# Performance work log

Measured on AMD Instinct MI355X. Metric: run time of the kernel, lower is better.

## Reference

```python
import jax, jax.numpy as jnp
import numpy as np
import math

B, N, D = 2, 4096, 1024
H, R, M = 16, 4, 8
BUCKET = 64

def setup_inputs() -> dict:
    key = jax.random.key(0)
    k1, k2, k3, k4, k5 = jax.random.split(key, 5)
    d = D // H
    return {
        "query": jax.random.normal(k1, (B, N, D), jnp.float32),
        "key": jax.random.normal(k2, (B, N, D), jnp.float32),
        "value": jax.random.normal(k3, (B, N, D), jnp.float32),
        "valence": jax.random.uniform(k4, (B,), jnp.float32),
        "hash_projections": jax.random.normal(k5, (R, H, d, M), jnp.float32),
        "valence_scale": jnp.ones((1,), jnp.float32),
    }

def reference(query, key, value, valence, hash_projections, valence_scale):
    b, n, dm = query.shape
    h = H
    d = dm // h
    r, _, _, m = hash_projections.shape
    c = n // BUCKET  # n_buckets (must divide exactly, matching torch view)
    # (B,N,D) -> (B,H,N,d)
    Q = query.reshape(b, n, h, d).transpose(0, 2, 1, 3)
    K = key.reshape(b, n, h, d).transpose(0, 2, 1, 3)
    V = value.reshape(b, n, h, d).transpose(0, 2, 1, 3)
    # LSH hash: argmax over M random projections per round -> (B,R,H,N)
    hashes = jnp.einsum('bhnd,rhdm->brhnm', Q, hash_projections)
    codes = jnp.argmax(hashes, axis=-1)
    # valence modulation (torch: scale.long().clamp(1, M); int truncation)
    scale = 1.0 + valence_scale[0] * valence.mean()
    scale_i = jnp.clip(scale.astype(jnp.int32), 1, m)
    codes = codes * scale_i
    # sort positions by hash code per (B,R,H)
    idx = jnp.argsort(codes, axis=-1)  # (B,R,H,N)
    idx_e = idx[..., None]  # (B,R,H,N,1), broadcasts over d
    K_sorted = jnp.take_along_axis(K[:, None], idx_e, axis=3)  # (B,R,H,N,d)
    V_sorted = jnp.take_along_axis(V[:, None], idx_e, axis=3)
    Kb = K_sorted.reshape(b, r, h, c, BUCKET, d)
    Vb = V_sorted.reshape(b, r, h, c, BUCKET, d)
    # NOTE: queries are bucketed in ORIGINAL order (faithful to source)
    Qb = Q.reshape(b, h, c, BUCKET, d)
    scores = jnp.einsum('bhcsd,brhced->brhcse', Qb, Kb) / math.sqrt(d)
    attn = jax.nn.softmax(scores, axis=-1)  # (B,R,H,C,S,E)
    outb = jnp.einsum('brhcse,brhced->brhcsd', attn, Vb)
    out = outb.reshape(b, r, h, n, d).mean(axis=1)  # average over hash rounds
    out = out.transpose(0, 2, 1, 3).reshape(b, n, dm)  # dropout is identity (eval)
    return out, attn.mean(axis=(1, 2))
```

## Files before the change

kernel.cpp:

```cpp
#include <hip/hip_runtime.h>
#include <hip/hip_bf16.h>

#define BB 2
#define NN 4096
#define DD 1024
#define HH 16
#define RR 4
#define MM 8
#define CC 64
#define DH 64
#define PAD 68

typedef __attribute__((ext_vector_type(8))) short bf16x8;
typedef __attribute__((ext_vector_type(8))) unsigned short ushort8;
typedef __attribute__((ext_vector_type(4))) float f32x4;
typedef unsigned long long u64;

__device__ __forceinline__ unsigned short f2bf(float x) {
  union { __hip_bfloat16 b; unsigned short u; } cv;
  cv.b = __float2bfloat16(x);
  return cv.u;
}
__device__ __forceinline__ int swz(int row, int colbyte) {
  return row * 128 + (colbyte ^ ((row & 7) << 4));
}
__device__ __forceinline__ bf16x8 pack8(float4 a, float4 b, float sc) {
  bf16x8 r;
  const float* pa = (const float*)&a;
  const float* pb = (const float*)&b;
#pragma unroll
  for (int j = 0; j < 4; ++j) {
    r[j] = (short)f2bf(pa[j] * sc);
    r[j + 4] = (short)f2bf(pb[j] * sc);
  }
  return r;
}
__device__ __forceinline__ void load_lds16(const void* g, void* l) {
  __builtin_amdgcn_global_load_lds(
      (const __attribute__((address_space(1))) unsigned*)g,
      (__attribute__((address_space(3))) unsigned*)l, 16, 0, 0);
}

__global__ __launch_bounds__(256) void k_cvt(const float* __restrict__ kmat,
                                             const float* __restrict__ vmat,
                                             unsigned short* __restrict__ kbf,
                                             unsigned short* __restrict__ vbf) {
  int bid = blockIdx.x;
  int b = bid >> 8;
  int n0 = (bid & 255) * 16;
  int tid = threadIdx.x;
  int h = tid >> 4, d4 = tid & 15;
#pragma unroll 4
  for (int it = 0; it < 16; ++it) {
    int row = n0 + it;
    size_t src = (size_t)(b * NN + row) * DD + tid * 4;
    float4 kv = *(const float4*)(kmat + src);
    float4 vv = *(const float4*)(vmat + src);
    size_t dst = ((size_t)(b * HH + h) * NN + row) * 64 + d4 * 4;
    const float* kf = (const float*)&kv;
    const float* vf = (const float*)&vv;
    u64 kp = (u64)f2bf(kf[0]) | ((u64)f2bf(kf[1]) << 16) |
             ((u64)f2bf(kf[2]) << 32) | ((u64)f2bf(kf[3]) << 48);
    u64 vp = (u64)f2bf(vf[0]) | ((u64)f2bf(vf[1]) << 16) |
             ((u64)f2bf(vf[2]) << 32) | ((u64)f2bf(vf[3]) << 48);
    *(u64*)(kbf + dst) = kp;
    *(u64*)(vbf + dst) = vp;
  }
}

__global__ __launch_bounds__(256) void k_hash(const float* __restrict__ q,
                                              const float* __restrict__ proj,
                                              int* __restrict__ codes) {
  int blk = blockIdx.x;
  int nc = blk & (CC - 1);
  int h = (blk >> 6) & (HH - 1);
  int b = blk >> 10;
  __shared__ float Qs[64][PAD];
  __shared__ float Ps[DH][MM];
  __shared__ float Ss[64][9];
  int tid = threadIdx.x;
  const float* qbase = q + ((size_t)(b * NN + nc * 64) * DD + h * DH);
  for (int f = tid; f < 1024; f += 256) {
    int row = f >> 4, c4 = f & 15;
    *(float4*)&Qs[row][c4 * 4] = *(const float4*)(qbase + (size_t)row * DD + c4 * 4);
  }
  int nl = tid >> 3, m = tid & 7;
  for (int r = 0; r < RR; ++r) {
    const float* pbase = proj + (size_t)(r * HH + h) * DH * MM;
    for (int f = tid; f < DH * MM / 4; f += 256)
      ((float4*)Ps)[f] = ((const float4*)pbase)[f];
    __syncthreads();
    float s0 = 0.f, s1 = 0.f;
#pragma unroll
    for (int kk = 0; kk < DH; ++kk) {
      float p = Ps[kk][m];
      s0 += Qs[nl][kk] * p;
      s1 += Qs[nl + 32][kk] * p;
    }
    Ss[nl][m] = s0;
    Ss[nl + 32][m] = s1;
    __syncthreads();
    if (tid < 64) {
      float best = Ss[tid][0];
      int bm = 0;
#pragma unroll
      for (int mm = 1; mm < MM; ++mm) {
        float vv = Ss[tid][mm];
        if (vv > best) { best = vv; bm = mm; }
      }
      codes[(size_t)((b * RR + r) * HH + h) * NN + nc * 64 + tid] = bm;
    }
    __syncthreads();
  }
}

__global__ __launch_bounds__(256) void k_sort(const int* __restrict__ codes,
                                              int* __restrict__ idxo) {
  int gblk = blockIdx.x;
  const int* cg = codes + (size_t)gblk * NN;
  int* ig = idxo + (size_t)gblk * NN;
  int tid = threadIdx.x, lane = tid & 63, w = tid >> 6;
  __shared__ u64 wtot[4][2];
  int myc[16];
#pragma unroll
  for (int qd = 0; qd < 4; ++qd) {
    int4 t4 = ((const int4*)(cg + tid * 16))[qd];
    myc[qd * 4 + 0] = t4.x; myc[qd * 4 + 1] = t4.y;
    myc[qd * 4 + 2] = t4.z; myc[qd * 4 + 3] = t4.w;
  }
  u64 c01 = 0, c23 = 0;
#pragma unroll
  for (int i = 0; i < 16; ++i) {
    int k = myc[i];
    u64 one = 1ull << (16 * (k & 3));
    if (k < 4) c01 += one; else c23 += one;
  }
  u64 i01 = c01, i23 = c23;
#pragma unroll
  for (int d = 1; d < 64; d <<= 1) {
    u64 t0 = __shfl_up(i01, d);
    u64 t1 = __shfl_up(i23, d);
    if (lane >= d) { i01 += t0; i23 += t1; }
  }
  if (lane == 63) { wtot[w][0] = i01; wtot[w][1] = i23; }
  __syncthreads();
  u64 base01 = 0, base23 = 0, g01 = 0, g23 = 0;
#pragma unroll
  for (int ww = 0; ww < 4; ++ww) {
    u64 a = wtot[ww][0], bq = wtot[ww][1];
    if (ww < w) { base01 += a; base23 += bq; }
    g01 += a; g23 += bq;
  }
  u64 p01 = g01 + (g01 << 16); p01 += (p01 << 32);
  u64 p23 = g23 + (g23 << 16); p23 += (p23 << 32);
  u64 cb01 = p01 << 16;
  u64 tot01 = (p01 >> 48) & 0xffffull;
  u64 cb23 = (p23 << 16) + tot01 * 0x0001000100010001ull;
  u64 o01 = cb01 + base01 + (i01 - c01);
  u64 o23 = cb23 + base23 + (i23 - c23);
#pragma unroll
  for (int i = 0; i < 16; ++i) {
    int k = myc[i];
    int sh = 16 * (k & 3);
    int off;
    if (k < 4) { off = (int)((o01 >> sh) & 0xffffull); o01 += 1ull << sh; }
    else       { off = (int)((o23 >> sh) & 0xffffull); o23 += 1ull << sh; }
    ig[off] = tid * 16 + i;
  }
}

__global__ __launch_bounds__(256, 4) void k_attn(const float* __restrict__ q,
                                                 const unsigned short* __restrict__ kbf,
                                                 const unsigned short* __restrict__ vbf,
                                                 const int* __restrict__ idxs,
                                                 float* __restrict__ out,
                                                 float* __restrict__ attn_part,
                                                 float* __restrict__ attn_out,
                                                 int atomic_attn) {
  __shared__ __align__(16) char KB[2][8192];
  __shared__ __align__(16) char VT[8192];
  __shared__ __align__(16) char PL[8192];
  __shared__ int sidx[RR][64];

  int bid = blockIdx.x;
  int blk = (bid & 7) * 256 + (bid >> 3);
  int cblk = blk & 63;
  int h = (blk >> 6) & 15;
  int b = blk >> 10;
  int tid = threadIdx.x;
  int lane = tid & 63;
  int w = tid >> 6;
  int g = lane >> 4;
  int cl = lane & 15;
  int e2 = tid & 31, dg = (tid >> 5) & 7;

  sidx[tid >> 6][tid & 63] =
      idxs[(size_t)((b * RR + (tid >> 6)) * HH + h) * NN + cblk * 64 + (tid & 63)];

  const char* kp = (const char*)(kbf + (size_t)(b * HH + h) * NN * 64);
  const unsigned short* vp = vbf + (size_t)(b * HH + h) * NN * 64;

  const float* qrow = q + (size_t)(b * NN + cblk * 64 + 16 * w + cl) * DD + h * DH;
  bf16x8 qh[2];
#pragma unroll
  for (int ks = 0; ks < 2; ++ks)
    qh[ks] = pack8(*(const float4*)(qrow + 32 * ks + 8 * g),
                   *(const float4*)(qrow + 32 * ks + 8 * g + 4), 0.125f);

  __syncthreads();

  {
    int row = sidx[0][16 * w + cl];
    const char* gs = kp + (size_t)row * 128 + g * 16;
    load_lds16(gs, KB[0] + w * 2048);
    load_lds16(gs + 64, KB[0] + w * 2048 + 1024);
    ushort8 v0r = *(const ushort8*)(vp + (size_t)sidx[0][2 * e2] * 64 + dg * 8);
    ushort8 v1r = *(const ushort8*)(vp + (size_t)sidx[0][2 * e2 + 1] * 64 + dg * 8);
#pragma unroll
    for (int j = 0; j < 8; ++j) {
      unsigned pk = (unsigned)(unsigned short)v0r[j] |
                    ((unsigned)(unsigned short)v1r[j] << 16);
      *(unsigned*)(VT + swz(8 * dg + j, 4 * e2)) = pk;
    }
  }
  __syncthreads();

  f32x4 acc_o[4];
  float attA[4][4];
#pragma unroll
  for (int t = 0; t < 4; ++t) {
    acc_o[t] = (f32x4){0.f, 0.f, 0.f, 0.f};
#pragma unroll
    for (int i = 0; i < 4; ++i) attA[t][i] = 0.f;
  }

#pragma unroll
  for (int r = 0; r < RR; ++r) {
    ushort8 n0r, n1r;
    if (r < RR - 1) {
      int row = sidx[r + 1][16 * w + cl];
      const char* gs = kp + (size_t)row * 128 + g * 16;
      load_lds16(gs, KB[(r + 1) & 1] + w * 2048);
      load_lds16(gs + 64, KB[(r + 1) & 1] + w * 2048 + 1024);
      n0r = *(const ushort8*)(vp + (size_t)sidx[r + 1][2 * e2] * 64 + dg * 8);
      n1r = *(const ushort8*)(vp + (size_t)sidx[r + 1][2 * e2 + 1] * 64 + dg * 8);
    }

    f32x4 s4[4];
#pragma unroll
    for (int t = 0; t < 4; ++t) s4[t] = (f32x4){0.f, 0.f, 0.f, 0.f};
    __builtin_amdgcn_s_setprio(1);
#pragma unroll
    for (int t = 0; t < 4; ++t)
#pragma unroll
      for (int ks = 0; ks < 2; ++ks) {
        bf16x8 kf = *(const bf16x8*)(KB[r & 1] + t * 2048 + ks * 1024 + g * 256 + cl * 16);
        s4[t] = __builtin_amdgcn_mfma_f32_16x16x32_bf16(kf, qh[ks], s4[t], 0, 0, 0);
      }
    __builtin_amdgcn_s_setprio(0);

    {
      f32x4 m4 = s4[0];
#pragma unroll
      for (int t = 1; t < 4; ++t)
#pragma unroll
        for (int i = 0; i < 4; ++i) m4[i] = fmaxf(m4[i], s4[t][i]);
      float mx = fmaxf(fmaxf(m4[0], m4[1]), fmaxf(m4[2], m4[3]));
      mx = fmaxf(mx, __shfl_xor(mx, 16));
      mx = fmaxf(mx, __shfl_xor(mx, 32));
      float sm = 0.f;
#pragma unroll
      for (int t = 0; t < 4; ++t)
#pragma unroll
        for (int i = 0; i < 4; ++i) {
          float e = __expf(s4[t][i] - mx);
          s4[t][i] = e;
          sm += e;
        }
      sm += __shfl_xor(sm, 16);
      sm += __shfl_xor(sm, 32);
      float inv = __builtin_amdgcn_rcpf(sm);
#pragma unroll
      for (int t = 0; t < 4; ++t)
#pragma unroll
        for (int i = 0; i < 4; ++i) {
          s4[t][i] *= inv;
          attA[t][i] += s4[t][i];
        }
    }

#pragma unroll
    for (int t = 0; t < 4; ++t) {
      u64 pk = (u64)f2bf(s4[t][0]) | ((u64)f2bf(s4[t][1]) << 16) |
               ((u64)f2bf(s4[t][2]) << 32) | ((u64)f2bf(s4[t][3]) << 48);
      *(u64*)(PL + w * 2048 + swz(cl, 32 * t + 8 * g)) = pk;
    }
    bf16x8 pa[2];
#pragma unroll
    for (int ks = 0; ks < 2; ++ks)
      pa[ks] = *(const bf16x8*)(PL + w * 2048 + swz(cl, 64 * ks + 16 * g));

    __builtin_amdgcn_s_setprio(1);
#pragma unroll
    for (int t = 0; t < 4; ++t)
#pragma unroll
      for (int ks = 0; ks < 2; ++ks) {
        bf16x8 vt = *(const bf16x8*)(VT + swz(16 * t + cl, ks * 64 + g * 16));
        acc_o[t] = __builtin_amdgcn_mfma_f32_16x16x32_bf16(vt, pa[ks], acc_o[t], 0, 0, 0);
      }
    __builtin_amdgcn_s_setprio(0);

    if (r < RR - 1) {
      __syncthreads();
#pragma unroll
      for (int j = 0; j < 8; ++j) {
        unsigned pk = (unsigned)(unsigned short)n0r[j] |
                      ((unsigned)(unsigned short)n1r[j] << 16);
        *(unsigned*)(VT + swz(8 * dg + j, 4 * e2)) = pk;
      }
      __syncthreads();
    }
  }

  int srow = 16 * w + cl;
  size_t ob = (size_t)(b * NN + cblk * 64 + srow) * DD + h * DH + 4 * g;
#pragma unroll
  for (int t = 0; t < 4; ++t) {
    float4 o = make_float4(acc_o[t][0] * 0.25f, acc_o[t][1] * 0.25f,
                           acc_o[t][2] * 0.25f, acc_o[t][3] * 0.25f);
    *(float4*)(out + ob + 16 * t) = o;
  }
  size_t ab = (((size_t)(b * HH + h) * CC + cblk) * 64 + srow) * 64 + 4 * g;
  if (atomic_attn) {
    const float sc = 1.f / (RR * HH);
    size_t abase = (((size_t)b * CC + cblk) * 64 + srow) * 64 + 4 * g;
#pragma unroll
    for (int t = 0; t < 4; ++t)
#pragma unroll
      for (int i = 0; i < 4; ++i)
        atomicAdd(attn_out + abase + 16 * t + i, attA[t][i] * sc);
  } else {
#pragma unroll
    for (int t = 0; t < 4; ++t) {
      float4 o = make_float4(attA[t][0], attA[t][1], attA[t][2], attA[t][3]);
      *(float4*)(attn_part + ab + 16 * t) = o;
    }
  }
}

__global__ __launch_bounds__(256) void k_attn_reduce(const float* __restrict__ part,
                                                     float* __restrict__ attn_out) {
  size_t o = (size_t)blockIdx.x * 256 + threadIdx.x;
  int se = (int)(o & 4095);
  size_t bc = o >> 12;
  int c = (int)(bc & (CC - 1));
  int b = (int)(bc >> 6);
  float s = 0.f;
  const float* p = part + ((size_t)b * HH * CC + c) * 4096 + se;
#pragma unroll
  for (int h = 0; h < HH; ++h) s += p[(size_t)h * CC * 4096];
  attn_out[o] = s * (1.f / (RR * HH));
}

extern "C" void kernel_launch(void* const* d_in, const int* in_sizes, int n_in,
                              void* d_out, int out_size, void* d_ws, size_t ws_size,
                              hipStream_t stream) {
  const float* q = (const float*)d_in[0];
  const float* k = (const float*)d_in[1];
  const float* v = (const float*)d_in[2];
  const float* proj = (const float*)d_in[4];
  float* out = (float*)d_out;
  float* attn_out = out + (size_t)BB * NN * DD;

  const size_t n_codes = (size_t)BB * RR * HH * NN;
  const size_t n_panel = (size_t)BB * HH * NN * 64;
  const size_t n_part  = (size_t)BB * HH * CC * 4096;

  int* codes = (int*)d_ws;
  int* idxs = codes + n_codes;
  unsigned short* kbf = (unsigned short*)(idxs + n_codes);
  unsigned short* vbf = kbf + n_panel;
  float* attn_part = (float*)(vbf + n_panel);

  size_t need_full = n_codes * 8 + n_panel * 4 + n_part * 4;
  int atomic_attn = (ws_size < need_full) ? 1 : 0;
  if (atomic_attn)
    hipMemsetAsync(attn_out, 0, (size_t)BB * CC * 4096 * sizeof(float), stream);

  k_cvt<<<BB * (NN / 16), 256, 0, stream>>>(k, v, kbf, vbf);
  k_hash<<<BB * HH * CC, 256, 0, stream>>>(q, proj, codes);
  k_sort<<<BB * RR * HH, 256, 0, stream>>>(codes, idxs);
  k_attn<<<BB * HH * CC, 256, 0, stream>>>(q, kbf, vbf, idxs, out, attn_part,
                                           attn_out, atomic_attn);
  if (!atomic_attn)
    k_attn_reduce<<<BB * CC * 4096 / 256, 256, 0, stream>>>(attn_part, attn_out);
}
```

Before: 90.70 us.

## Feed P straight from registers into 16x16x16 MFMA and restructure K/V conversion

The attention kernel no longer stages the softmax probabilities through an LDS buffer. It packs them into bf16x4 registers and feeds them directly to 16x16x16 bf16 MFMAs, whose operand layout matches the score accumulator. V transpose reads switch to an 8-byte swizzle to suit the smaller loads. Dropping the PL buffer lowers LDS use and the launch-bounds occupancy hint rises from 4 to 6 blocks. The K/V bf16 conversion kernel is rewritten so each block handles one tensor, with 16-byte stores that loop over heads. The trade-off is twice as many MFMA instructions of half the K depth, plus possible register pressure at the higher occupancy target.

Result: slower. 213.4 us (+135.3%).

```diff
diff --git a/kernel.cpp b/kernel.cpp
--- a/kernel.cpp
+++ b/kernel.cpp
@@ -12,6 +12,7 @@
 #define PAD 68
 
 typedef __attribute__((ext_vector_type(8))) short bf16x8;
+typedef __attribute__((ext_vector_type(4))) short bf16x4;
 typedef __attribute__((ext_vector_type(8))) unsigned short ushort8;
 typedef __attribute__((ext_vector_type(4))) float f32x4;
 typedef unsigned long long u64;
@@ -24,6 +25,9 @@
 __device__ __forceinline__ int swz(int row, int colbyte) {
   return row * 128 + (colbyte ^ ((row & 7) << 4));
 }
+__device__ __forceinline__ int swz8(int row, int colbyte) {
+  return row * 128 + (colbyte ^ ((row & 15) << 3));
+}
 __device__ __forceinline__ bf16x8 pack8(float4 a, float4 b, float sc) {
   bf16x8 r;
   const float* pa = (const float*)&a;
@@ -39,6 +43,17 @@
   __builtin_amdgcn_global_load_lds(
       (const __attribute__((address_space(1))) unsigned*)g,
       (__attribute__((address_space(3))) unsigned*)l, 16, 0, 0);
+}
+__device__ __forceinline__ f32x4 mfma16(bf16x4 a, bf16x4 b, f32x4 c) {
+#if __has_builtin(__builtin_amdgcn_mfma_f32_16x16x16bf16_1k)
+  return __builtin_amdgcn_mfma_f32_16x16x16bf16_1k(a, b, c, 0, 0, 0);
+#elif __has_builtin(__builtin_amdgcn_mfma_f32_16x16x16_bf16)
+  return __builtin_amdgcn_mfma_f32_16x16x16_bf16(a, b, c, 0, 0, 0);
+#else
+  f32x4 d;
+  asm("v_mfma_f32_16x16x16_bf16 %0, %1, %2, %3" : "=v"(d) : "v"(a), "v"(b), "v"(c));
+  return d;
+#endif
 }
 
 __global__ __launch_bounds__(256) void k_cvt(const float* __restrict__ kmat,
@@ -46,25 +61,29 @@
                                              unsigned short* __restrict__ kbf,
                                              unsigned short* __restrict__ vbf) {
   int bid = blockIdx.x;
-  int b = bid >> 8;
-  int n0 = (bid & 255) * 16;
+  int sel = bid >> 8;
+  int rest = bid & 255;
+  int b = rest >> 7;
+  int chunk = rest & 127;
+  const float* src = sel ? vmat : kmat;
+  unsigned short* dst = sel ? vbf : kbf;
   int tid = threadIdx.x;
-  int h = tid >> 4, d4 = tid & 15;
+  int row = chunk * 32 + (tid >> 3), oct = tid & 7;
+  const float* s0 = src + (size_t)(b * NN + row) * DD + oct * 8;
+  unsigned short* d0 = dst + (size_t)b * HH * NN * 64 + (size_t)row * 64 + oct * 8;
 #pragma unroll 4
-  for (int it = 0; it < 16; ++it) {
-    int row = n0 + it;
-    size_t src = (size_t)(b * NN + row) * DD + tid * 4;
-    float4 kv = *(const float4*)(kmat + src);
-    float4 vv = *(const float4*)(vmat + src);
-    size_t dst = ((size_t)(b * HH + h) * NN + row) * 64 + d4 * 4;
-    const float* kf = (const float*)&kv;
-    const float* vf = (const float*)&vv;
-    u64 kp = (u64)f2bf(kf[0]) | ((u64)f2bf(kf[1]) << 16) |
-             ((u64)f2bf(kf[2]) << 32) | ((u64)f2bf(kf[3]) << 48);
-    u64 vp = (u64)f2bf(vf[0]) | ((u64)f2bf(vf[1]) << 16) |
-             ((u64)f2bf(vf[2]) << 32) | ((u64)f2bf(vf[3]) << 48);
-    *(u64*)(kbf + dst) = kp;
-    *(u64*)(vbf + dst) = vp;
+  for (int h = 0; h < HH; ++h) {
+    float4 a = *(const float4*)(s0 + h * 64);
+    float4 c = *(const float4*)(s0 + h * 64 + 4);
+    const float* af = (const float*)&a;
+    const float* cf = (const float*)&c;
+    ushort8 o;
+#pragma unroll
+    for (int j = 0; j < 4; ++j) {
+      o[j] = f2bf(af[j]);
+      o[j + 4] = f2bf(cf[j]);
+    }
+    *(ushort8*)(d0 + (size_t)h * NN * 64) = o;
   }
 }
 
@@ -169,7 +188,7 @@
   }
 }
 
-__global__ __launch_bounds__(256, 4) void k_attn(const float* __restrict__ q,
+__global__ __launch_bounds__(256, 6) void k_attn(const float* __restrict__ q,
                                                  const unsigned short* __restrict__ kbf,
                                                  const unsigned short* __restrict__ vbf,
                                                  const int* __restrict__ idxs,
@@ -179,7 +198,6 @@
                                                  int atomic_attn) {
   __shared__ __align__(16) char KB[2][8192];
   __shared__ __align__(16) char VT[8192];
-  __shared__ __align__(16) char PL[8192];
   __shared__ int sidx[RR][64];
 
   int bid = blockIdx.x;
@@ -220,7 +238,7 @@
     for (int j = 0; j < 8; ++j) {
       unsigned pk = (unsigned)(unsigned short)v0r[j] |
                     ((unsigned)(unsigned short)v1r[j] << 16);
-      *(unsigned*)(VT + swz(8 * dg + j, 4 * e2)) = pk;
+      *(unsigned*)(VT + swz8(8 * dg + j, 4 * e2)) = pk;
     }
   }
   __syncthreads();
@@ -289,25 +307,26 @@
         }
     }
 
+    bf16x4 pb[4];
 #pragma unroll
     for (int t = 0; t < 4; ++t) {
-      u64 pk = (u64)f2bf(s4[t][0]) | ((u64)f2bf(s4[t][1]) << 16) |
-               ((u64)f2bf(s4[t][2]) << 32) | ((u64)f2bf(s4[t][3]) << 48);
-      *(u64*)(PL + w * 2048 + swz(cl, 32 * t + 8 * g)) = pk;
-    }
-    bf16x8 pa[2];
-#pragma unroll
-    for (int ks = 0; ks < 2; ++ks)
-      pa[ks] = *(const bf16x8*)(PL + w * 2048 + swz(cl, 64 * ks + 16 * g));
+      bf16x4 pv;
+#pragma unroll
+      for (int i = 0; i < 4; ++i) pv[i] = (short)f2bf(s4[t][i]);
+      pb[t] = pv;
+    }
 
     __builtin_amdgcn_s_setprio(1);
 #pragma unroll
-    for (int t = 0; t < 4; ++t)
-#pragma unroll
-      for (int ks = 0; ks < 2; ++ks) {
-        bf16x8 vt = *(const bf16x8*)(VT + swz(16 * t + cl, ks * 64 + g * 16));
-        acc_o[t] = __builtin_amdgcn_mfma_f32_16x16x32_bf16(vt, pa[ks], acc_o[t], 0, 0, 0);
-      }
+    for (int td = 0; td < 4; ++td) {
+      bf16x4 va[4];
+#pragma unroll
+      for (int ec = 0; ec < 4; ++ec)
+        va[ec] = *(const bf16x4*)(VT + swz8(16 * td + cl, 32 * ec + 8 * g));
+#pragma unroll
+      for (int ec = 0; ec < 4; ++ec)
+        acc_o[td] = mfma16(va[ec], pb[ec], acc_o[td]);
+    }
     __builtin_amdgcn_s_setprio(0);
 
     if (r < RR - 1) {
@@ -316,7 +335,7 @@
       for (int j = 0; j < 8; ++j) {
         unsigned pk = (unsigned)(unsigned short)n0r[j] |
                       ((unsigned)(unsigned short)n1r[j] << 16);
-        *(unsigned*)(VT + swz(8 * dg + j, 4 * e2)) = pk;
+        *(unsigned*)(VT + swz8(8 * dg + j, 4 * e2)) = pk;
       }
       __syncthreads();
     }
@@ -387,7 +406,7 @@
   if (atomic_attn)
     hipMemsetAsync(attn_out, 0, (size_t)BB * CC * 4096 * sizeof(float), stream);
 
-  k_cvt<<<BB * (NN / 16), 256, 0, stream>>>(k, v, kbf, vbf);
+  k_cvt<<<2 * BB * (NN / 32), 256, 0, stream>>>(k, v, kbf, vbf);
   k_hash<<<BB * HH * CC, 256, 0, stream>>>(q, proj, codes);
   k_sort<<<BB * RR * HH, 256, 0, stream>>>(codes, idxs);
   k_attn<<<BB * HH * CC, 256, 0, stream>>>(q, kbf, vbf, idxs, out, attn_part,
```

## Restructure K/V bf16 conversion and stage K through registers instead of direct LDS loads

Applied to the files above, without the earlier changes.

The conversion kernel now splits K and V into separate blocks. Each thread converts 8 contiguous floats per head and writes a 16-byte vector, replacing the old interleaved 8-byte stores, which should give more coalesced panel writes. In the attention kernel, the double-buffered K tile filled by global_load_lds is replaced by a single buffer. K rows are prefetched into registers and written to LDS after the barrier, the same way V is handled. This cuts LDS usage by 8KB per block, which may raise occupancy, but K loads now take VGPRs and stores go through the shader instead of the async LDS path.

Result: slower. 93.17 us, median of 2 (+2.7%).

```diff
diff --git a/kernel.cpp b/kernel.cpp
--- a/kernel.cpp
+++ b/kernel.cpp
@@ -35,36 +35,35 @@
   }
   return r;
 }
-__device__ __forceinline__ void load_lds16(const void* g, void* l) {
-  __builtin_amdgcn_global_load_lds(
-      (const __attribute__((address_space(1))) unsigned*)g,
-      (__attribute__((address_space(3))) unsigned*)l, 16, 0, 0);
-}
 
 __global__ __launch_bounds__(256) void k_cvt(const float* __restrict__ kmat,
                                              const float* __restrict__ vmat,
                                              unsigned short* __restrict__ kbf,
                                              unsigned short* __restrict__ vbf) {
   int bid = blockIdx.x;
-  int b = bid >> 8;
-  int n0 = (bid & 255) * 16;
+  int sel = bid >> 8;
+  int rest = bid & 255;
+  int b = rest >> 7;
+  int chunk = rest & 127;
+  const float* src = sel ? vmat : kmat;
+  unsigned short* dst = sel ? vbf : kbf;
   int tid = threadIdx.x;
-  int h = tid >> 4, d4 = tid & 15;
+  int row = chunk * 32 + (tid >> 3), oct = tid & 7;
+  const float* s0 = src + (size_t)(b * NN + row) * DD + oct * 8;
+  unsigned short* d0 = dst + (size_t)b * HH * NN * 64 + (size_t)row * 64 + oct * 8;
 #pragma unroll 4
-  for (int it = 0; it < 16; ++it) {
-    int row = n0 + it;
-    size_t src = (size_t)(b * NN + row) * DD + tid * 4;
-    float4 kv = *(const float4*)(kmat + src);
-    float4 vv = *(const float4*)(vmat + src);
-    size_t dst = ((size_t)(b * HH + h) * NN + row) * 64 + d4 * 4;
-    const float* kf = (const float*)&kv;
-    const float* vf = (const float*)&vv;
-    u64 kp = (u64)f2bf(kf[0]) | ((u64)f2bf(kf[1]) << 16) |
-             ((u64)f2bf(kf[2]) << 32) | ((u64)f2bf(kf[3]) << 48);
-    u64 vp = (u64)f2bf(vf[0]) | ((u64)f2bf(vf[1]) << 16) |
-             ((u64)f2bf(vf[2]) << 32) | ((u64)f2bf(vf[3]) << 48);
-    *(u64*)(kbf + dst) = kp;
-    *(u64*)(vbf + dst) = vp;
+  for (int h = 0; h < HH; ++h) {
+    float4 a = *(const float4*)(s0 + h * 64);
+    float4 c = *(const float4*)(s0 + h * 64 + 4);
+    const float* af = (const float*)&a;
+    const float* cf = (const float*)&c;
+    ushort8 o;
+#pragma unroll
+    for (int j = 0; j < 4; ++j) {
+      o[j] = f2bf(af[j]);
+      o[j + 4] = f2bf(cf[j]);
+    }
+    *(ushort8*)(d0 + (size_t)h * NN * 64) = o;
   }
 }
 
@@ -177,7 +176,7 @@
                                                  float* __restrict__ attn_part,
                                                  float* __restrict__ attn_out,
                                                  int atomic_attn) {
-  __shared__ __align__(16) char KB[2][8192];
+  __shared__ __align__(16) char KB[8192];
   __shared__ __align__(16) char VT[8192];
   __shared__ __align__(16) char PL[8192];
   __shared__ int sidx[RR][64];
@@ -197,7 +196,7 @@
   sidx[tid >> 6][tid & 63] =
       idxs[(size_t)((b * RR + (tid >> 6)) * HH + h) * NN + cblk * 64 + (tid & 63)];
 
-  const char* kp = (const char*)(kbf + (size_t)(b * HH + h) * NN * 64);
+  const unsigned short* kp = kbf + (size_t)(b * HH + h) * NN * 64;
   const unsigned short* vp = vbf + (size_t)(b * HH + h) * NN * 64;
 
   const float* qrow = q + (size_t)(b * NN + cblk * 64 + 16 * w + cl) * DD + h * DH;
@@ -210,12 +209,13 @@
   __syncthreads();
 
   {
-    int row = sidx[0][16 * w + cl];
-    const char* gs = kp + (size_t)row * 128 + g * 16;
-    load_lds16(gs, KB[0] + w * 2048);
-    load_lds16(gs + 64, KB[0] + w * 2048 + 1024);
+    const unsigned short* kr = kp + (size_t)sidx[0][16 * w + cl] * 64 + g * 8;
+    ushort8 k0a = *(const ushort8*)kr;
+    ushort8 k0b = *(const ushort8*)(kr + 32);
     ushort8 v0r = *(const ushort8*)(vp + (size_t)sidx[0][2 * e2] * 64 + dg * 8);
     ushort8 v1r = *(const ushort8*)(vp + (size_t)sidx[0][2 * e2 + 1] * 64 + dg * 8);
+    *(ushort8*)(KB + w * 2048 + g * 256 + cl * 16) = k0a;
+    *(ushort8*)(KB + w * 2048 + 1024 + g * 256 + cl * 16) = k0b;
 #pragma unroll
     for (int j = 0; j < 8; ++j) {
       unsigned pk = (unsigned)(unsigned short)v0r[j] |
@@ -236,12 +236,11 @@
 
 #pragma unroll
   for (int r = 0; r < RR; ++r) {
-    ushort8 n0r, n1r;
+    ushort8 kna, knb, n0r, n1r;
     if (r < RR - 1) {
-      int row = sidx[r + 1][16 * w + cl];
-      const char* gs = kp + (size_t)row * 128 + g * 16;
-      load_lds16(gs, KB[(r + 1) & 1] + w * 2048);
-      load_lds16(gs + 64, KB[(r + 1) & 1] + w * 2048 + 1024);
+      const unsigned short* krn = kp + (size_t)sidx[r + 1][16 * w + cl] * 64 + g * 8;
+      kna = *(const ushort8*)krn;
+      knb = *(const ushort8*)(krn + 32);
       n0r = *(const ushort8*)(vp + (size_t)sidx[r + 1][2 * e2] * 64 + dg * 8);
       n1r = *(const ushort8*)(vp + (size_t)sidx[r + 1][2 * e2 + 1] * 64 + dg * 8);
     }
@@ -254,7 +253,7 @@
     for (int t = 0; t < 4; ++t)
 #pragma unroll
       for (int ks = 0; ks < 2; ++ks) {
-        bf16x8 kf = *(const bf16x8*)(KB[r & 1] + t * 2048 + ks * 1024 + g * 256 + cl * 16);
+        bf16x8 kf = *(const bf16x8*)(KB + t * 2048 + ks * 1024 + g * 256 + cl * 16);
         s4[t] = __builtin_amdgcn_mfma_f32_16x16x32_bf16(kf, qh[ks], s4[t], 0, 0, 0);
       }
     __builtin_amdgcn_s_setprio(0);
@@ -312,6 +311,8 @@
 
     if (r < RR - 1) {
       __syncthreads();
+      *(ushort8*)(KB + w * 2048 + g * 256 + cl * 16) = kna;
+      *(ushort8*)(KB + w * 2048 + 1024 + g * 256 + cl * 16) = knb;
 #pragma unroll
       for (int j = 0; j < 8; ++j) {
         unsigned pk = (unsigned)(unsigned short)n0r[j] |
@@ -387,7 +388,7 @@
   if (atomic_attn)
     hipMemsetAsync(attn_out, 0, (size_t)BB * CC * 4096 * sizeof(float), stream);
 
-  k_cvt<<<BB * (NN / 16), 256, 0, stream>>>(k, v, kbf, vbf);
+  k_cvt<<<2 * BB * (NN / 32), 256, 0, stream>>>(k, v, kbf, vbf);
   k_hash<<<BB * HH * CC, 256, 0, stream>>>(q, proj, codes);
   k_sort<<<BB * RR * HH, 256, 0, stream>>>(codes, idxs);
   k_attn<<<BB * HH * CC, 256, 0, stream>>>(q, kbf, vbf, idxs, out, attn_part,
```
